# Optimization experiments

Measured on AMD Instinct MI355X. Metric: run time of the kernel, lower is better.

Reference implementation:

```python
import jax, jax.numpy as jnp
import numpy as np

D_ENC = 512
D_DEC = 512
JOINT = 512
VOCAB = 1024


def setup_inputs() -> dict:
    key = jax.random.key(0)
    ks = jax.random.split(key, 7)
    B, T, U = 4, 256, 64
    s_enc = 1.0 / np.sqrt(D_ENC)
    s_dec = 1.0 / np.sqrt(D_DEC)
    s_out = 1.0 / np.sqrt(JOINT)
    return {
        "encoder_out": jax.random.normal(ks[0], (B, T, 1, D_ENC), dtype=jnp.float32),
        "decoder_out": jax.random.normal(ks[1], (B, 1, U, D_DEC), dtype=jnp.float32),
        # torch.nn.Linear stores weight as (out, in); uniform(-1/sqrt(in), 1/sqrt(in))
        "W_enc": jax.random.uniform(ks[2], (JOINT, D_ENC), jnp.float32, -s_enc, s_enc),
        "b_enc": jax.random.uniform(ks[3], (JOINT,), jnp.float32, -s_enc, s_enc),
        "W_dec": jax.random.uniform(ks[4], (JOINT, D_DEC), jnp.float32, -s_dec, s_dec),
        "W_out": jax.random.uniform(ks[5], (VOCAB, JOINT), jnp.float32, -s_out, s_out),
        "b_out": jax.random.uniform(ks[6], (VOCAB,), jnp.float32, -s_out, s_out),
    }


def reference(encoder_out, decoder_out, W_enc, b_enc, W_dec, W_out, b_out):
    # Project each side in its small shape first (B,T,1,J) and (B,1,U,J),
    # then broadcast-add over (T,U), tanh, output GEMM -> (B,T,U,V).
    enc = jnp.einsum("btud,jd->btuj", encoder_out, W_enc) + b_enc  # (B,T,1,J)
    dec = jnp.einsum("btud,jd->btuj", decoder_out, W_dec)          # (B,1,U,J)
    h = jnp.tanh(enc + dec)                                        # (B,T,U,J)
    return jnp.einsum("btuj,vj->btuv", h, W_out) + b_out           # (B,T,U,V)
```

## Files before the change

kernel.cpp:

```cpp
#include <hip/hip_runtime.h>
#include <hip/hip_bf16.h>


typedef __attribute__((ext_vector_type(8))) short short8;
typedef __attribute__((ext_vector_type(4))) float f32x4;
typedef __attribute__((ext_vector_type(4))) unsigned short u16x4;

#define SZ0 524288
#define SZ1 131072
#define SZ2 262144
#define SZ3 512
#define SZ4 262144
#define SZ5 524288
#define SZ6 1024
#define CU0 0
#define CU1 524288
#define CU2 655360
#define CU3 917504
#define CU4 918016
#define CU5 1180160
#define CU6 1704448
#define CTOT 1705472

__global__ void detect_kernel(const void* p0, const void* p1, const void* p2,
                              const void* p3, const void* p4, const void* p5,
                              const void* p6, int* flags) {
  const void* ps[7] = {p0, p1, p2, p3, p4, p5, p6};
  const int sz[7] = {SZ0, SZ1, SZ2, SZ3, SZ4, SZ5, SZ6};
  const int w = threadIdx.x >> 6;
  const int l = threadIdx.x & 63;
  if (w >= 7) return;
  const unsigned short* u = (const unsigned short*)ps[w];
  const int lim = sz[w] < 1024 ? sz[w] : 1024;
  int bad = 0;
  for (int j = l; j < lim; j += 64) {
    const unsigned e = (u[j] >> 7) & 0xFFu;
    if (e >= 0x8Eu) bad = 1;
  }
  const unsigned long long b = __ballot(bad);
  if (l == 0) flags[w] = (b != 0ULL) ? 1 : 0;
}

__global__ __launch_bounds__(256) void convert_kernel(
    const void* p0, const void* p1, const void* p2, const void* p3,
    const void* p4, const void* p5, const void* p6,
    const int* __restrict__ flags, __hip_bfloat16* __restrict__ dst) {
  const int gid = blockIdx.x * 256 + threadIdx.x;
  if (gid >= CTOT) return;
  int t, local;
  const void* p;
  if (gid < CU1)      { t = 0; local = gid - CU0; p = p0; }
  else if (gid < CU2) { t = 1; local = gid - CU1; p = p1; }
  else if (gid < CU3) { t = 2; local = gid - CU2; p = p2; }
  else if (gid < CU4) { t = 3; local = gid - CU3; p = p3; }
  else if (gid < CU5) { t = 4; local = gid - CU4; p = p4; }
  else if (gid < CU6) { t = 5; local = gid - CU5; p = p5; }
  else                { t = 6; local = gid - CU6; p = p6; }
  __hip_bfloat16 v;
  if (flags[t])
    v = __float2bfloat16(((const float*)p)[local]);
  else
    v = ((const __hip_bfloat16*)p)[local];
  dst[gid] = v;
}

template <bool OUT_BF16>
__global__ __launch_bounds__(256) void gemm_bt(
    const __hip_bfloat16* __restrict__ A, const __hip_bfloat16* __restrict__ Bw,
    const __hip_bfloat16* __restrict__ bias, void* __restrict__ Cv,
    int M, int N, int K) {
  __shared__ __align__(16) __hip_bfloat16 sA[128 * 64];
  __shared__ __align__(16) __hip_bfloat16 sB[128 * 64];

  const int tid = threadIdx.x;
  const int w = tid >> 6;
  const int l = tid & 63;
  const int ntiles = N >> 7;
  const int mt = blockIdx.x / ntiles;
  const int nt = blockIdx.x % ntiles;
  const int m0 = mt << 7;
  const int n0 = nt << 7;
  const int wm = (w >> 1) << 6;
  const int wn = (w & 1) << 6;
  const int r16 = l & 15;
  const int q = l >> 4;

  f32x4 acc[4][4] = {};

  const int srow_in = l >> 3;
  const int scol = (l & 7) << 3;

  for (int k0 = 0; k0 < K; k0 += 64) {
#pragma unroll
    for (int i = 0; i < 4; ++i) {
      const int c = (w << 2) + i;
      const int row = (c << 3) + srow_in;
      const __hip_bfloat16* gA = A + (size_t)(m0 + row) * K + k0 + scol;
      const __hip_bfloat16* gB = Bw + (size_t)(n0 + row) * K + k0 + scol;
      __builtin_amdgcn_global_load_lds(
          (const __attribute__((address_space(1))) void*)gA,
          (__attribute__((address_space(3))) void*)(sA + (c << 9) + (l << 3)),
          16, 0, 0);
      __builtin_amdgcn_global_load_lds(
          (const __attribute__((address_space(1))) void*)gB,
          (__attribute__((address_space(3))) void*)(sB + (c << 9) + (l << 3)),
          16, 0, 0);
    }
    __syncthreads();

#pragma unroll
    for (int kk = 0; kk < 2; ++kk) {
      const int kc = (kk << 5) + (q << 3);
      short8 af[4], bf[4];
#pragma unroll
      for (int mi = 0; mi < 4; ++mi)
        af[mi] = *(const short8*)(sA + (wm + (mi << 4) + r16) * 64 + kc);
#pragma unroll
      for (int ni = 0; ni < 4; ++ni)
        bf[ni] = *(const short8*)(sB + (wn + (ni << 4) + r16) * 64 + kc);
#pragma unroll
      for (int mi = 0; mi < 4; ++mi)
#pragma unroll
        for (int ni = 0; ni < 4; ++ni)
          acc[mi][ni] = __builtin_amdgcn_mfma_f32_16x16x32_bf16(
              af[mi], bf[ni], acc[mi][ni], 0, 0, 0);
    }
    __syncthreads();
  }

  __hip_bfloat16* outB = (__hip_bfloat16*)Cv;
  float* outF = (float*)Cv;
#pragma unroll
  for (int ni = 0; ni < 4; ++ni) {
    const int col = n0 + wn + (ni << 4) + r16;
    const float bc = bias ? __bfloat162float(bias[col]) : 0.0f;
#pragma unroll
    for (int mi = 0; mi < 4; ++mi) {
      const int rowb = m0 + wm + (mi << 4) + (q << 2);
#pragma unroll
      for (int i = 0; i < 4; ++i) {
        const float v = acc[mi][ni][i] + bc;
        if (OUT_BF16)
          outB[(size_t)(rowb + i) * N + col] = __float2bfloat16(v);
        else
          outF[(size_t)(rowb + i) * N + col] = v;
      }
    }
  }
}

__global__ __launch_bounds__(256) void h_kernel(
    const float* __restrict__ Pe, const float* __restrict__ Pd,
    __hip_bfloat16* __restrict__ H, int total4) {
  const int idx = blockIdx.x * blockDim.x + threadIdx.x;
  if (idx >= total4) return;
  const int m = idx >> 7;
  const int k = (idx & 127) << 2;
  const int e = m >> 6;
  const int d = ((m >> 14) << 6) + (m & 63);
  const f32x4 pe = *(const f32x4*)(Pe + (size_t)e * 512 + k);
  const f32x4 pd = *(const f32x4*)(Pd + (size_t)d * 512 + k);
  u16x4 o;
#pragma unroll
  for (int j = 0; j < 4; ++j) {
    const float s = pe[j] + pd[j];
    const float t = 1.0f - 2.0f / (__expf(2.0f * s) + 1.0f);
    const __hip_bfloat16 hb = __float2bfloat16(t);
    o[j] = *(const unsigned short*)&hb;
  }
  *(u16x4*)(H + (size_t)idx * 4) = o;
}

__global__ __launch_bounds__(256) void gemm_fused(
    const float* __restrict__ Pe, const float* __restrict__ Pd,
    const __hip_bfloat16* __restrict__ Bw,
    const __hip_bfloat16* __restrict__ bias, float* __restrict__ out) {
  __shared__ __align__(16) __hip_bfloat16 sA[128 * 64];
  __shared__ __align__(16) __hip_bfloat16 sB[128 * 64];
  const int tid = threadIdx.x;
  const int w = tid >> 6;
  const int l = tid & 63;
  const int mt = blockIdx.x >> 3;
  const int nt = blockIdx.x & 7;
  const int m0 = mt << 7;
  const int n0 = nt << 7;
  const int wm = (w >> 1) << 6;
  const int wn = (w & 1) << 6;
  const int r16 = l & 15;
  const int q = l >> 4;
  f32x4 acc[4][4] = {};
  const int arow = tid >> 3;
  const int acol = (tid & 7) << 3;

  for (int k0 = 0; k0 < 512; k0 += 64) {
#pragma unroll
    for (int i = 0; i < 4; ++i) {
      const int c = (w << 2) + i;
      const int row = (c << 3) + (l >> 3);
      const int col = (l & 7) << 3;
      __builtin_amdgcn_global_load_lds(
          (const __attribute__((address_space(1))) void*)(
              Bw + (size_t)(n0 + row) * 512 + k0 + col),
          (__attribute__((address_space(3))) void*)(sB + (c << 9) + (l << 3)),
          16, 0, 0);
    }
#pragma unroll
    for (int c2 = 0; c2 < 4; ++c2) {
      const int row = arow + (c2 << 5);
      const int m = m0 + row;
      const int e = m >> 6;
      const int dd = ((m >> 14) << 6) | (m & 63);
      const float* pe = Pe + (size_t)e * 512 + k0 + acol;
      const float* pd = Pd + (size_t)dd * 512 + k0 + acol;
      const f32x4 e0 = *(const f32x4*)pe, e1 = *(const f32x4*)(pe + 4);
      const f32x4 g0 = *(const f32x4*)pd, g1 = *(const f32x4*)(pd + 4);
      short8 hv;
#pragma unroll
      for (int j = 0; j < 4; ++j) {
        float s = e0[j] + g0[j];
        float t = 1.0f - 2.0f / (__expf(2.0f * s) + 1.0f);
        __hip_bfloat16 hb = __float2bfloat16(t);
        hv[j] = *(const short*)&hb;
        s = e1[j] + g1[j];
        t = 1.0f - 2.0f / (__expf(2.0f * s) + 1.0f);
        hb = __float2bfloat16(t);
        hv[4 + j] = *(const short*)&hb;
      }
      *(short8*)(sA + row * 64 + acol) = hv;
    }
    __syncthreads();
#pragma unroll
    for (int kk = 0; kk < 2; ++kk) {
      const int kc = (kk << 5) + (q << 3);
      short8 af[4], bf[4];
#pragma unroll
      for (int mi = 0; mi < 4; ++mi)
        af[mi] = *(const short8*)(sA + (wm + (mi << 4) + r16) * 64 + kc);
#pragma unroll
      for (int ni = 0; ni < 4; ++ni)
        bf[ni] = *(const short8*)(sB + (wn + (ni << 4) + r16) * 64 + kc);
#pragma unroll
      for (int mi = 0; mi < 4; ++mi)
#pragma unroll
        for (int ni = 0; ni < 4; ++ni)
          acc[mi][ni] = __builtin_amdgcn_mfma_f32_16x16x32_bf16(
              af[mi], bf[ni], acc[mi][ni], 0, 0, 0);
    }
    __syncthreads();
  }

#pragma unroll
  for (int ni = 0; ni < 4; ++ni) {
    const int col = n0 + wn + (ni << 4) + r16;
    const float bc = __bfloat162float(bias[col]);
#pragma unroll
    for (int mi = 0; mi < 4; ++mi) {
      const int rowb = m0 + wm + (mi << 4) + (q << 2);
#pragma unroll
      for (int i = 0; i < 4; ++i)
        out[(size_t)(rowb + i) * 1024 + col] = acc[mi][ni][i] + bc;
    }
  }
}

extern "C" void kernel_launch(void* const* d_in, const int* in_sizes, int n_in,
                              void* d_out, int out_size, void* d_ws,
                              size_t ws_size, hipStream_t stream) {
  char* ws = (char*)d_ws;
  int* flags = (int*)ws;
  __hip_bfloat16* cp = (__hip_bfloat16*)(ws + 256);
  float* Pe = (float*)(ws + (4ull << 20));
  float* Pd = (float*)(ws + (6ull << 20));
  __hip_bfloat16* H = (__hip_bfloat16*)(ws + (8ull << 20));
  const bool haveH = ws_size >= (72ull << 20);

  detect_kernel<<<dim3(1), dim3(512), 0, stream>>>(
      d_in[0], d_in[1], d_in[2], d_in[3], d_in[4], d_in[5], d_in[6], flags);
  convert_kernel<<<dim3((CTOT + 255) / 256), dim3(256), 0, stream>>>(
      d_in[0], d_in[1], d_in[2], d_in[3], d_in[4], d_in[5], d_in[6], flags, cp);

  const __hip_bfloat16* enc_c = cp + CU0;
  const __hip_bfloat16* dec_c = cp + CU1;
  const __hip_bfloat16* Wenc_c = cp + CU2;
  const __hip_bfloat16* benc_c = cp + CU3;
  const __hip_bfloat16* Wdec_c = cp + CU4;
  const __hip_bfloat16* Wout_c = cp + CU5;
  const __hip_bfloat16* bout_c = cp + CU6;

  gemm_bt<false><<<dim3(32), dim3(256), 0, stream>>>(enc_c, Wenc_c, benc_c, Pe,
                                                     1024, 512, 512);
  gemm_bt<false><<<dim3(8), dim3(256), 0, stream>>>(dec_c, Wdec_c, nullptr, Pd,
                                                    256, 512, 512);
  if (haveH) {
    h_kernel<<<dim3(32768), dim3(256), 0, stream>>>(Pe, Pd, H, 8388608);
    gemm_bt<false><<<dim3(4096), dim3(256), 0, stream>>>(
        H, Wout_c, bout_c, d_out, 65536, 1024, 512);
  } else {
    gemm_fused<<<dim3(4096), dim3(256), 0, stream>>>(
        Pe, Pd, Wout_c, bout_c, (float*)d_out);
  }
}
```

Measured before the change: 431.4 us.

## Always use fused tanh-GEMM path and merge projection GEMMs into one launch

Drops the materialized H buffer path (separate tanh kernel writing bf16 H, then a GEMM reading it) and always runs the fused kernel, which computes tanh(Pe+Pd) while staging the A tile. The encoder and decoder projection GEMMs are also merged into one 40-block launch. This removes a large intermediate write/read and two launches, at the cost of recomputing tanh per N-tile inside the GEMM.

```diff
diff --git a/kernel.cpp b/kernel.cpp
--- a/kernel.cpp
+++ b/kernel.cpp
@@ -4,7 +4,6 @@
 
 typedef __attribute__((ext_vector_type(8))) short short8;
 typedef __attribute__((ext_vector_type(4))) float f32x4;
-typedef __attribute__((ext_vector_type(4))) unsigned short u16x4;
 
 #define SZ0 524288
 #define SZ1 131072
@@ -64,20 +63,17 @@
   dst[gid] = v;
 }
 
-template <bool OUT_BF16>
-__global__ __launch_bounds__(256) void gemm_bt(
+__device__ __forceinline__ void gemm_bt_body(
     const __hip_bfloat16* __restrict__ A, const __hip_bfloat16* __restrict__ Bw,
-    const __hip_bfloat16* __restrict__ bias, void* __restrict__ Cv,
-    int M, int N, int K) {
-  __shared__ __align__(16) __hip_bfloat16 sA[128 * 64];
-  __shared__ __align__(16) __hip_bfloat16 sB[128 * 64];
-
+    const __hip_bfloat16* __restrict__ bias, float* __restrict__ C,
+    int M, int N, int K, int bid,
+    __hip_bfloat16* sA, __hip_bfloat16* sB) {
   const int tid = threadIdx.x;
   const int w = tid >> 6;
   const int l = tid & 63;
   const int ntiles = N >> 7;
-  const int mt = blockIdx.x / ntiles;
-  const int nt = blockIdx.x % ntiles;
+  const int mt = bid / ntiles;
+  const int nt = bid % ntiles;
   const int m0 = mt << 7;
   const int n0 = nt << 7;
   const int wm = (w >> 1) << 6;
@@ -128,8 +124,6 @@
     __syncthreads();
   }
 
-  __hip_bfloat16* outB = (__hip_bfloat16*)Cv;
-  float* outF = (float*)Cv;
 #pragma unroll
   for (int ni = 0; ni < 4; ++ni) {
     const int col = n0 + wn + (ni << 4) + r16;
@@ -138,37 +132,23 @@
     for (int mi = 0; mi < 4; ++mi) {
       const int rowb = m0 + wm + (mi << 4) + (q << 2);
 #pragma unroll
-      for (int i = 0; i < 4; ++i) {
-        const float v = acc[mi][ni][i] + bc;
-        if (OUT_BF16)
-          outB[(size_t)(rowb + i) * N + col] = __float2bfloat16(v);
-        else
-          outF[(size_t)(rowb + i) * N + col] = v;
-      }
-    }
-  }
-}
-
-__global__ __launch_bounds__(256) void h_kernel(
-    const float* __restrict__ Pe, const float* __restrict__ Pd,
-    __hip_bfloat16* __restrict__ H, int total4) {
-  const int idx = blockIdx.x * blockDim.x + threadIdx.x;
-  if (idx >= total4) return;
-  const int m = idx >> 7;
-  const int k = (idx & 127) << 2;
-  const int e = m >> 6;
-  const int d = ((m >> 14) << 6) + (m & 63);
-  const f32x4 pe = *(const f32x4*)(Pe + (size_t)e * 512 + k);
-  const f32x4 pd = *(const f32x4*)(Pd + (size_t)d * 512 + k);
-  u16x4 o;
-#pragma unroll
-  for (int j = 0; j < 4; ++j) {
-    const float s = pe[j] + pd[j];
-    const float t = 1.0f - 2.0f / (__expf(2.0f * s) + 1.0f);
-    const __hip_bfloat16 hb = __float2bfloat16(t);
-    o[j] = *(const unsigned short*)&hb;
-  }
-  *(u16x4*)(H + (size_t)idx * 4) = o;
+      for (int i = 0; i < 4; ++i)
+        C[(size_t)(rowb + i) * N + col] = acc[mi][ni][i] + bc;
+    }
+  }
+}
+
+__global__ __launch_bounds__(256) void proj_kernel(
+    const __hip_bfloat16* __restrict__ enc, const __hip_bfloat16* __restrict__ Wenc,
+    const __hip_bfloat16* __restrict__ benc,
+    const __hip_bfloat16* __restrict__ dec, const __hip_bfloat16* __restrict__ Wdec,
+    float* __restrict__ Pe, float* __restrict__ Pd) {
+  __shared__ __align__(16) __hip_bfloat16 sA[128 * 64];
+  __shared__ __align__(16) __hip_bfloat16 sB[128 * 64];
+  if (blockIdx.x < 32)
+    gemm_bt_body(enc, Wenc, benc, Pe, 1024, 512, 512, blockIdx.x, sA, sB);
+  else
+    gemm_bt_body(dec, Wdec, nullptr, Pd, 256, 512, 512, blockIdx.x - 32, sA, sB);
 }
 
 __global__ __launch_bounds__(256) void gemm_fused(
@@ -271,8 +251,6 @@
   __hip_bfloat16* cp = (__hip_bfloat16*)(ws + 256);
   float* Pe = (float*)(ws + (4ull << 20));
   float* Pd = (float*)(ws + (6ull << 20));
-  __hip_bfloat16* H = (__hip_bfloat16*)(ws + (8ull << 20));
-  const bool haveH = ws_size >= (72ull << 20);
 
   detect_kernel<<<dim3(1), dim3(512), 0, stream>>>(
       d_in[0], d_in[1], d_in[2], d_in[3], d_in[4], d_in[5], d_in[6], flags);
@@ -287,16 +265,8 @@
   const __hip_bfloat16* Wout_c = cp + CU5;
   const __hip_bfloat16* bout_c = cp + CU6;
 
-  gemm_bt<false><<<dim3(32), dim3(256), 0, stream>>>(enc_c, Wenc_c, benc_c, Pe,
-                                                     1024, 512, 512);
-  gemm_bt<false><<<dim3(8), dim3(256), 0, stream>>>(dec_c, Wdec_c, nullptr, Pd,
-                                                    256, 512, 512);
-  if (haveH) {
-    h_kernel<<<dim3(32768), dim3(256), 0, stream>>>(Pe, Pd, H, 8388608);
-    gemm_bt<false><<<dim3(4096), dim3(256), 0, stream>>>(
-        H, Wout_c, bout_c, d_out, 65536, 1024, 512);
-  } else {
-    gemm_fused<<<dim3(4096), dim3(256), 0, stream>>>(
-        Pe, Pd, Wout_c, bout_c, (float*)d_out);
-  }
-}
+  proj_kernel<<<dim3(40), dim3(256), 0, stream>>>(enc_c, Wenc_c, benc_c,
+                                                  dec_c, Wdec_c, Pe, Pd);
+  gemm_fused<<<dim3(4096), dim3(256), 0, stream>>>(
+      Pe, Pd, Wout_c, bout_c, (float*)d_out);
+}
```

Result: slower. 465.4 us (+7.9%).
